# Optimization experiments

Hardware: AMD Instinct MI355X
Metric: run time of the kernel (lower is better)

## Reference

```python
import jax, jax.numpy as jnp
import numpy as np

F, G, S, E, P, B, T = 1024, 512, 512, 256, 8, 256, 256

def _gru(x, h, W_ih, W_hh, b_ih, b_hh):
    # torch.nn.GRUCell math; gate order r, z, n
    gi = x @ W_ih.T + b_ih
    gh = h @ W_hh.T + b_hh
    ir, iz, inn = jnp.split(gi, 3, axis=1)
    hr, hz, hn = jnp.split(gh, 3, axis=1)
    r = jax.nn.sigmoid(ir + hr)
    z = jax.nn.sigmoid(iz + hz)
    n = jnp.tanh(inn + r * hn)
    return (1.0 - z) * n + z * h

def setup_inputs() -> dict:
    key = jax.random.key(0)
    ks = jax.random.split(key, 16)
    feature_ = jax.random.normal(ks[0], (B, F), dtype=jnp.float32)
    spk_id = jax.random.randint(ks[1], (B,), 0, P)
    speaker_mask = jax.nn.one_hot(spk_id, P, dtype=jnp.float32)
    global_history = jax.random.normal(ks[2], (T, B, G), dtype=jnp.float32)
    speaker0 = jax.random.normal(ks[3], (B, P, S), dtype=jnp.float32)
    emotion0 = jax.random.normal(ks[4], (B, E), dtype=jnp.float32)
    sc = 0.05
    return {
        "feature_": feature_, "speaker_mask": speaker_mask,
        "global_history": global_history, "speaker0": speaker0, "emotion0": emotion0,
        "Wg_ih": jax.random.normal(ks[5], (3 * G, F + S)) * sc,
        "Wg_hh": jax.random.normal(ks[6], (3 * G, G)) * sc,
        "bg_ih": jnp.zeros((3 * G,)), "bg_hh": jnp.zeros((3 * G,)),
        "Wp_ih": jax.random.normal(ks[7], (3 * S, F + G)) * sc,
        "Wp_hh": jax.random.normal(ks[8], (3 * S, S)) * sc,
        "bp_ih": jnp.zeros((3 * S,)), "bp_hh": jnp.zeros((3 * S,)),
        "We_ih": jax.random.normal(ks[9], (3 * E, S)) * sc,
        "We_hh": jax.random.normal(ks[10], (3 * E, E)) * sc,
        "be_ih": jnp.zeros((3 * E,)), "be_hh": jnp.zeros((3 * E,)),
        "attn_W": jax.random.normal(ks[11], (G, F)) * sc,
    }

def reference(feature_, speaker_mask, global_history, speaker0, emotion0,
              Wg_ih, Wg_hh, bg_ih, bg_hh,
              Wp_ih, Wp_hh, bp_ih, bp_hh,
              We_ih, We_hh, be_ih, be_hh, attn_W):
    b = feature_.shape[0]
    p = speaker_mask.shape[1]
    spk_id = jnp.argmax(speaker_mask, axis=1)                      # (B,)
    rows = jnp.arange(b)
    sel0 = speaker0[rows, spk_id]                                   # select_parties -> (B, S)
    feature_speak = jnp.concatenate([feature_, sel0], axis=1)       # (B, F+S)
    global_state = _gru(feature_speak, global_history[-1], Wg_ih, Wg_hh, bg_ih, bg_hh)
    # attention over global history (T > 0 path); dropout = identity (eval)
    x_ = feature_ @ attn_W.T                                        # (B, G)
    alpha = jax.nn.softmax(jnp.einsum('bg,tbg->bt', x_, global_history), axis=1)
    context = jnp.einsum('bt,tbg->bg', alpha, global_history)       # (B, G)
    feature_context = jnp.concatenate([feature_, context], axis=1)  # (B, F+G)
    fc = jnp.broadcast_to(feature_context[:, None, :], (b, p, feature_context.shape[1]))
    fc = fc.reshape(b * p, -1)
    parties_state = _gru(fc, speaker0.reshape(b * p, -1), Wp_ih, Wp_hh, bp_ih, bp_hh)
    parties_state = parties_state.reshape(b, p, -1)                 # (B, P, S)
    m = speaker_mask[:, :, None]
    speaker = speaker0 * (1.0 - m) + parties_state * m
    parties = speaker[rows, spk_id]                                 # (B, S)
    emotion = _gru(parties, emotion0, We_ih, We_hh, be_ih, be_hh)
    return emotion, global_state, speaker
```

## Files before the change

kernel.cpp:

```cpp
#include <hip/hip_runtime.h>
#include <hip/hip_bf16.h>
#include <math.h>

#define BB 256
#define FF 1024
#define GG 512
#define SS 512
#define EE 256
#define PP 8
#define TT 256

typedef __attribute__((ext_vector_type(8))) short bs8;
typedef __attribute__((ext_vector_type(4))) float f32x4;

__device__ __forceinline__ float sigmoidf_(float x) { return 1.0f / (1.0f + expf(-x)); }

__device__ __forceinline__ short f2bf(float f) {
    union { float f; unsigned u; } v; v.f = f;
    unsigned r = v.u + 0x7FFFu + ((v.u >> 16) & 1u);
    return (short)(r >> 16);
}

union BPack { bs8 s; __hip_bfloat162 h[4]; };

__device__ __forceinline__ bs8 ld8cvt(const float* p) {
    float4 a = *(const float4*)p, b = *(const float4*)(p + 4);
    BPack u;
    u.h[0] = __float22bfloat162_rn({a.x, a.y});
    u.h[1] = __float22bfloat162_rn({a.z, a.w});
    u.h[2] = __float22bfloat162_rn({b.x, b.y});
    u.h[3] = __float22bfloat162_rn({b.z, b.w});
    return u.s;
}
__device__ __forceinline__ void ld8split(const float* p, bs8& ho, bs8& lo) {
    float4 a = *(const float4*)p, b = *(const float4*)(p + 4);
    float v[8] = {a.x, a.y, a.z, a.w, b.x, b.y, b.z, b.w};
    BPack uh, ul;
#pragma unroll
    for (int j = 0; j < 4; ++j) {
        __hip_bfloat162 h2 = __float22bfloat162_rn({v[2*j], v[2*j+1]});
        uh.h[j] = h2;
        float r0 = v[2*j]   - __low2float(h2);
        float r1 = v[2*j+1] - __high2float(h2);
        ul.h[j] = __float22bfloat162_rn({r0, r1});
    }
    ho = uh.s; lo = ul.s;
}

#define OWG_IH 0L
#define OWG_HH 2359296L
#define OWP_IH 3145728L
#define OWP_HH 5505024L
#define OWE_IH 6291456L
#define OWE_HH 6684672L
#define WTOT   6881280L

#define MB0 0
#define MB1 3360
#define MB2 3616
#define MB3 3744
#define MB4 3808
#define MB5 3840
#define MB6 4096
#define MBE 5120

__global__ __launch_bounds__(256) void k_mega(
        const float* __restrict__ Wg_ih, const float* __restrict__ Wg_hh,
        const float* __restrict__ Wp_ih, const float* __restrict__ Wp_hh,
        const float* __restrict__ We_ih, const float* __restrict__ We_hh,
        const float* __restrict__ attn_W, const float* __restrict__ feature_,
        const float* __restrict__ h_g, const float* __restrict__ emotion0,
        const float* __restrict__ mask, const float* __restrict__ sp0,
        short* __restrict__ Wbf, short* __restrict__ awhi, short* __restrict__ awlo,
        short* __restrict__ xg, short* __restrict__ fhi, short* __restrict__ flo,
        short* __restrict__ hg_bf, short* __restrict__ emo_bf, short* __restrict__ sel0_bf,
        float* __restrict__ sel0, int* __restrict__ spk, float* __restrict__ speaker_out) {
    int blk = blockIdx.x, tid = threadIdx.x;
    if (blk < MB1) {
        long i = (long)blk * 2048 + tid * 8;
        const float* src; long base;
        if      (i < OWG_HH) { src = Wg_ih; base = OWG_IH; }
        else if (i < OWP_IH) { src = Wg_hh; base = OWG_HH; }
        else if (i < OWP_HH) { src = Wp_ih; base = OWP_IH; }
        else if (i < OWE_IH) { src = Wp_hh; base = OWP_HH; }
        else if (i < OWE_HH) { src = We_ih; base = OWE_IH; }
        else                 { src = We_hh; base = OWE_HH; }
        *(bs8*)(Wbf + i) = ld8cvt(src + (i - base));
    } else if (blk < MB2) {
        long i = (long)(blk - MB1) * 2048 + tid * 8;
        bs8 h, l;
        ld8split(attn_W + i, h, l);
        *(bs8*)(awhi + i) = h;
        *(bs8*)(awlo + i) = l;
    } else if (blk < MB3) {
        long i = (long)(blk - MB2) * 2048 + tid * 8;
        bs8 h, l;
        ld8split(feature_ + i, h, l);
        *(bs8*)(fhi + i) = h;
        *(bs8*)(flo + i) = l;
        long b = i >> 10, c = i & 1023;
        *(bs8*)(xg + b * 1536 + c) = h;
    } else if (blk < MB4) {
        long i = (long)(blk - MB3) * 2048 + tid * 8;
        *(bs8*)(hg_bf + i) = ld8cvt(h_g + i);
    } else if (blk < MB5) {
        long i = (long)(blk - MB4) * 2048 + tid * 8;
        *(bs8*)(emo_bf + i) = ld8cvt(emotion0 + i);
    } else if (blk < MB6) {
        int b = blk - MB5;
        __shared__ int sid;
        if (tid == 0) {
            int best = 0; float bv = mask[b * PP];
            for (int p = 1; p < PP; ++p) { float v = mask[b * PP + p]; if (v > bv) { bv = v; best = p; } }
            sid = best; spk[b] = best;
        }
        __syncthreads();
        const float* src = sp0 + ((size_t)b * PP + sid) * SS;
        for (int j = tid; j < SS; j += 256) {
            float v = src[j];
            sel0[(size_t)b * SS + j] = v;
            short h = f2bf(v);
            sel0_bf[(size_t)b * SS + j] = h;
            xg[(size_t)b * 1536 + FF + j] = h;
        }
    } else {
        size_t i = ((size_t)(blk - MB6) * 256 + tid) * 4;
        *(float4*)(speaker_out + i) = *(const float4*)(sp0 + i);
    }
}

struct GDesc {
    const short *A, *A2, *W, *Wl;
    float* C;
    int lda, lda2, kb, ldw, woff, ldc, K, nbn, flags;
};
struct GBatch {
    GDesc d[6];
    int start[7];
    int ng;
};

__global__ __launch_bounds__(256) void k_bgemm(GBatch gb) {
    __shared__ __align__(16) short Ash[64 * 64], Bsh[64 * 64];
    __shared__ __align__(16) short Asl[64 * 64], Bsl[64 * 64];

    int bid = blockIdx.x;
    int g = 0;
    while (g + 1 < gb.ng && bid >= gb.start[g + 1]) ++g;
    GDesc d = gb.d[g];
    int local = bid - gb.start[g];
    int bn = local % d.nbn, bm = local / d.nbn;
    const bool split = (d.flags & 1) != 0;

    const int tid = threadIdx.x;
    const int lane = tid & 63, wid = tid >> 6;
    const int wr = wid >> 1, wc = wid & 1;
    const int r0 = tid >> 3, c0 = tid & 7;
    const int r1 = r0 + 32;
    const int la = lane & 15, lk = lane >> 4;
    const int sw = la & 7;

    f32x4 acc[2][2] = {};

    for (int k0 = 0; k0 < d.K; k0 += 64) {
        bs8 ah0, ah1, bh0, bh1, al0, al1, bl0, bl1;
        if (split) {
            size_t oa0 = (size_t)(bm * 64 + r0) * d.lda + k0 + c0 * 8;
            size_t oa1 = (size_t)(bm * 64 + r1) * d.lda + k0 + c0 * 8;
            size_t ow0 = (size_t)(bn * 64 + r0) * d.ldw + d.woff + k0 + c0 * 8;
            size_t ow1 = (size_t)(bn * 64 + r1) * d.ldw + d.woff + k0 + c0 * 8;
            ah0 = *(const bs8*)(d.A + oa0);  ah1 = *(const bs8*)(d.A + oa1);
            al0 = *(const bs8*)(d.A2 + oa0); al1 = *(const bs8*)(d.A2 + oa1);
            bh0 = *(const bs8*)(d.W + ow0);  bh1 = *(const bs8*)(d.W + ow1);
            bl0 = *(const bs8*)(d.Wl + ow0); bl1 = *(const bs8*)(d.Wl + ow1);
        } else {
            const short* Ab; int alda;
            if (k0 < d.kb) { Ab = d.A + k0; alda = d.lda; }
            else           { Ab = d.A2 + (k0 - d.kb); alda = d.lda2; }
            ah0 = *(const bs8*)(Ab + (size_t)(bm * 64 + r0) * alda + c0 * 8);
            ah1 = *(const bs8*)(Ab + (size_t)(bm * 64 + r1) * alda + c0 * 8);
            bh0 = *(const bs8*)(d.W + (size_t)(bn * 64 + r0) * d.ldw + d.woff + k0 + c0 * 8);
            bh1 = *(const bs8*)(d.W + (size_t)(bn * 64 + r1) * d.ldw + d.woff + k0 + c0 * 8);
        }
        __syncthreads();
        *(bs8*)(Ash + r0 * 64 + ((c0 ^ (r0 & 7)) * 8)) = ah0;
        *(bs8*)(Ash + r1 * 64 + ((c0 ^ (r1 & 7)) * 8)) = ah1;
        *(bs8*)(Bsh + r0 * 64 + ((c0 ^ (r0 & 7)) * 8)) = bh0;
        *(bs8*)(Bsh + r1 * 64 + ((c0 ^ (r1 & 7)) * 8)) = bh1;
        if (split) {
            *(bs8*)(Asl + r0 * 64 + ((c0 ^ (r0 & 7)) * 8)) = al0;
            *(bs8*)(Asl + r1 * 64 + ((c0 ^ (r1 & 7)) * 8)) = al1;
            *(bs8*)(Bsl + r0 * 64 + ((c0 ^ (r0 & 7)) * 8)) = bl0;
            *(bs8*)(Bsl + r1 * 64 + ((c0 ^ (r1 & 7)) * 8)) = bl1;
        }
        __syncthreads();
#pragma unroll
        for (int kk = 0; kk < 2; ++kk) {
            int slot = kk * 4 + lk;
            int off = (slot ^ sw) * 8;
            bs8 a0 = *(const bs8*)(Ash + (wr * 32 + la) * 64      + off);
            bs8 a1 = *(const bs8*)(Ash + (wr * 32 + 16 + la) * 64 + off);
            bs8 b0 = *(const bs8*)(Bsh + (wc * 32 + la) * 64      + off);
            bs8 b1 = *(const bs8*)(Bsh + (wc * 32 + 16 + la) * 64 + off);
            acc[0][0] = __builtin_amdgcn_mfma_f32_16x16x32_bf16(a0, b0, acc[0][0], 0, 0, 0);
            acc[0][1] = __builtin_amdgcn_mfma_f32_16x16x32_bf16(a0, b1, acc[0][1], 0, 0, 0);
            acc[1][0] = __builtin_amdgcn_mfma_f32_16x16x32_bf16(a1, b0, acc[1][0], 0, 0, 0);
            acc[1][1] = __builtin_amdgcn_mfma_f32_16x16x32_bf16(a1, b1, acc[1][1], 0, 0, 0);
            if (split) {
                bs8 xl0 = *(const bs8*)(Asl + (wr * 32 + la) * 64      + off);
                bs8 xl1 = *(const bs8*)(Asl + (wr * 32 + 16 + la) * 64 + off);
                bs8 yl0 = *(const bs8*)(Bsl + (wc * 32 + la) * 64      + off);
                bs8 yl1 = *(const bs8*)(Bsl + (wc * 32 + 16 + la) * 64 + off);
                acc[0][0] = __builtin_amdgcn_mfma_f32_16x16x32_bf16(a0, yl0, acc[0][0], 0, 0, 0);
                acc[0][0] = __builtin_amdgcn_mfma_f32_16x16x32_bf16(xl0, b0, acc[0][0], 0, 0, 0);
                acc[0][1] = __builtin_amdgcn_mfma_f32_16x16x32_bf16(a0, yl1, acc[0][1], 0, 0, 0);
                acc[0][1] = __builtin_amdgcn_mfma_f32_16x16x32_bf16(xl0, b1, acc[0][1], 0, 0, 0);
                acc[1][0] = __builtin_amdgcn_mfma_f32_16x16x32_bf16(a1, yl0, acc[1][0], 0, 0, 0);
                acc[1][0] = __builtin_amdgcn_mfma_f32_16x16x32_bf16(xl1, b0, acc[1][0], 0, 0, 0);
                acc[1][1] = __builtin_amdgcn_mfma_f32_16x16x32_bf16(a1, yl1, acc[1][1], 0, 0, 0);
                acc[1][1] = __builtin_amdgcn_mfma_f32_16x16x32_bf16(xl1, b1, acc[1][1], 0, 0, 0);
            }
        }
    }

    const int rowb = (lane >> 4) * 4, coln = lane & 15;
    const bool accum = (d.flags & 2) != 0;
#pragma unroll
    for (int i = 0; i < 2; ++i)
#pragma unroll
    for (int j = 0; j < 2; ++j)
#pragma unroll
    for (int r = 0; r < 4; ++r) {
        int row = bm * 64 + wr * 32 + i * 16 + rowb + r;
        int col = bn * 64 + wc * 32 + j * 16 + coln;
        size_t idx = (size_t)row * d.ldc + col;
        if (accum) d.C[idx] += acc[i][j][r];
        else       d.C[idx]  = acc[i][j][r];
    }
}

__global__ __launch_bounds__(256) void k_scores(const float* __restrict__ x_,
                                                const float* __restrict__ gh,
                                                float* __restrict__ scores) {
    int task = blockIdx.x * 4 + (threadIdx.x >> 6);
    int lane = threadIdx.x & 63;
    int b = task & (BB - 1), t = task >> 8;
    const float* row = gh + ((size_t)t * BB + b) * GG + lane * 8;
    const float* xb  = x_ + (size_t)b * GG + lane * 8;
    float4 v1 = *(const float4*)row;
    float4 v2 = *(const float4*)(row + 4);
    float4 x1 = *(const float4*)xb;
    float4 x2 = *(const float4*)(xb + 4);
    float p = v1.x*x1.x + v1.y*x1.y + v1.z*x1.z + v1.w*x1.w
            + v2.x*x2.x + v2.y*x2.y + v2.z*x2.z + v2.w*x2.w;
#pragma unroll
    for (int off = 32; off; off >>= 1) p += __shfl_xor(p, off);
    if (lane == 0) scores[b * TT + t] = p;
}

__global__ __launch_bounds__(1024) void k_softctx(const float* __restrict__ scores,
                                                  const float* __restrict__ gh,
                                                  short* __restrict__ ctx_bf) {
    int b = blockIdx.x, tid = threadIdx.x;
    __shared__ float sal[TT];
    __shared__ float red[TT];
    __shared__ float part[16][GG];

    float v = 0.f;
    if (tid < TT) { v = scores[b * TT + tid]; red[tid] = v; }
    __syncthreads();
    for (int off = 128; off; off >>= 1) {
        if (tid < off) red[tid] = fmaxf(red[tid], red[tid + off]);
        __syncthreads();
    }
    float m = red[0];
    __syncthreads();
    float e = 0.f;
    if (tid < TT) { e = expf(v - m); red[tid] = e; }
    __syncthreads();
    for (int off = 128; off; off >>= 1) {
        if (tid < off) red[tid] += red[tid + off];
        __syncthreads();
    }
    if (tid < TT) sal[tid] = e / red[0];
    __syncthreads();

    int w = tid >> 6, lane = tid & 63;
    float acc[8] = {};
    for (int it = 0; it < 16; ++it) {
        int t = w * 16 + it;
        float a = sal[t];
        const float* row = gh + ((size_t)t * BB + b) * GG + lane * 8;
        float4 v1 = *(const float4*)row;
        float4 v2 = *(const float4*)(row + 4);
        acc[0] += a * v1.x; acc[1] += a * v1.y; acc[2] += a * v1.z; acc[3] += a * v1.w;
        acc[4] += a * v2.x; acc[5] += a * v2.y; acc[6] += a * v2.z; acc[7] += a * v2.w;
    }
#pragma unroll
    for (int e2 = 0; e2 < 8; ++e2) part[w][lane * 8 + e2] = acc[e2];
    __syncthreads();
    if (tid < GG) {
        float s = 0.f;
#pragma unroll
        for (int w2 = 0; w2 < 16; ++w2) s += part[w2][tid];
        ctx_bf[(size_t)b * GG + tid] = f2bf(s);
    }
}

__global__ __launch_bounds__(256) void k_gru2(
        const float* __restrict__ gi_g, const float* __restrict__ gh_g,
        const float* __restrict__ bg_ih, const float* __restrict__ bg_hh,
        const float* __restrict__ hg, float* __restrict__ global_out,
        const float* __restrict__ gi_p, const float* __restrict__ gh_p,
        const float* __restrict__ bp_ih, const float* __restrict__ bp_hh,
        const float* __restrict__ sel0, const int* __restrict__ spk,
        short* __restrict__ par_bf, float* __restrict__ speaker_out) {
    int idx = blockIdx.x * 256 + threadIdx.x;
    if (idx < BB * GG) {
        int b = idx / GG, j = idx - b * GG;
        const float* gib = gi_g + (size_t)b * 3 * GG;
        const float* ghb = gh_g + (size_t)b * 3 * GG;
        float r = sigmoidf_(gib[j] + bg_ih[j] + ghb[j] + bg_hh[j]);
        float z = sigmoidf_(gib[GG + j] + bg_ih[GG + j] + ghb[GG + j] + bg_hh[GG + j]);
        float n = tanhf(gib[2*GG + j] + bg_ih[2*GG + j] + r * (ghb[2*GG + j] + bg_hh[2*GG + j]));
        global_out[idx] = (1.0f - z) * n + z * hg[idx];
    } else {
        idx -= BB * GG;
        int b = idx / SS, j = idx - b * SS;
        const float* gib = gi_p + (size_t)b * 3 * SS;
        const float* ghb = gh_p + (size_t)b * 3 * SS;
        float r = sigmoidf_(gib[j] + bp_ih[j] + ghb[j] + bp_hh[j]);
        float z = sigmoidf_(gib[SS + j] + bp_ih[SS + j] + ghb[SS + j] + bp_hh[SS + j]);
        float n = tanhf(gib[2*SS + j] + bp_ih[2*SS + j] + r * (ghb[2*SS + j] + bp_hh[2*SS + j]));
        float o = (1.0f - z) * n + z * sel0[idx];
        par_bf[idx] = f2bf(o);
        speaker_out[((size_t)b * PP + spk[b]) * SS + j] = o;
    }
}

__global__ __launch_bounds__(256) void k_gru(const float* __restrict__ gi, const float* __restrict__ gh,
                                             const float* __restrict__ bih, const float* __restrict__ bhh,
                                             const float* __restrict__ h,
                                             float* __restrict__ out, int H) {
    int idx = blockIdx.x * 256 + threadIdx.x;
    int b = idx / H, j = idx - b * H;
    const float* gib = gi + (size_t)b * 3 * H;
    const float* ghb = gh + (size_t)b * 3 * H;
    float r = sigmoidf_(gib[j] + bih[j] + ghb[j] + bhh[j]);
    float z = sigmoidf_(gib[H + j] + bih[H + j] + ghb[H + j] + bhh[H + j]);
    float n = tanhf(gib[2 * H + j] + bih[2 * H + j] + r * (ghb[2 * H + j] + bhh[2 * H + j]));
    out[idx] = (1.0f - z) * n + z * h[idx];
}

extern "C" void kernel_launch(void* const* d_in, const int* in_sizes, int n_in,
                              void* d_out, int out_size, void* d_ws, size_t ws_size,
                              hipStream_t stream) {
    const float* feature_ = (const float*)d_in[0];
    const float* mask     = (const float*)d_in[1];
    const float* ghist    = (const float*)d_in[2];
    const float* speaker0 = (const float*)d_in[3];
    const float* emotion0 = (const float*)d_in[4];
    const float* Wg_ih    = (const float*)d_in[5];
    const float* Wg_hh    = (const float*)d_in[6];
    const float* bg_ih    = (const float*)d_in[7];
    const float* bg_hh    = (const float*)d_in[8];
    const float* Wp_ih    = (const float*)d_in[9];
    const float* Wp_hh    = (const float*)d_in[10];
    const float* bp_ih    = (const float*)d_in[11];
    const float* bp_hh    = (const float*)d_in[12];
    const float* We_ih    = (const float*)d_in[13];
    const float* We_hh    = (const float*)d_in[14];
    const float* be_ih    = (const float*)d_in[15];
    const float* be_hh    = (const float*)d_in[16];
    const float* attn_W   = (const float*)d_in[17];

    float* out = (float*)d_out;
    float* emotion_out = out;
    float* global_out  = out + (size_t)BB * EE;
    float* speaker_out = global_out + (size_t)BB * GG;

    char* cur = (char*)d_ws;
    short* Wbf     = (short*)cur; cur += (size_t)WTOT * 2;
    short* awhi    = (short*)cur; cur += (size_t)GG * FF * 2;
    short* awlo    = (short*)cur; cur += (size_t)GG * FF * 2;
    short* xg      = (short*)cur; cur += (size_t)BB * 1536 * 2;
    short* fhi     = (short*)cur; cur += (size_t)BB * FF * 2;
    short* flo     = (short*)cur; cur += (size_t)BB * FF * 2;
    short* hg_bf   = (short*)cur; cur += (size_t)BB * GG * 2;
    short* emo_bf  = (short*)cur; cur += (size_t)BB * EE * 2;
    short* sel0_bf = (short*)cur; cur += (size_t)BB * SS * 2;
    short* ctx_bf  = (short*)cur; cur += (size_t)BB * GG * 2;
    short* par_bf  = (short*)cur; cur += (size_t)BB * SS * 2;

    float* sel0    = (float*)cur; cur += (size_t)BB * SS * 4;
    float* x_      = (float*)cur; cur += (size_t)BB * GG * 4;
    float* scores  = (float*)cur; cur += (size_t)BB * TT * 4;
    float* gi_g    = (float*)cur; cur += (size_t)BB * 3 * GG * 4;
    float* gh_g    = (float*)cur; cur += (size_t)BB * 3 * GG * 4;
    float* gi_p    = (float*)cur; cur += (size_t)BB * 3 * SS * 4;
    float* gh_p    = (float*)cur; cur += (size_t)BB * 3 * SS * 4;
    float* gi_e    = (float*)cur; cur += (size_t)BB * 3 * EE * 4;
    float* gh_e    = (float*)cur; cur += (size_t)BB * 3 * EE * 4;
    int*   spk     = (int*)cur;   cur += 256 * 4;

    const float* h_g = ghist + (size_t)(TT - 1) * BB * GG;

    short* Wg_ih_bf = Wbf + OWG_IH;
    short* Wg_hh_bf = Wbf + OWG_HH;
    short* Wp_ih_bf = Wbf + OWP_IH;
    short* Wp_hh_bf = Wbf + OWP_HH;
    short* We_ih_bf = Wbf + OWE_IH;
    short* We_hh_bf = Wbf + OWE_HH;

    k_mega<<<MBE, 256, 0, stream>>>(Wg_ih, Wg_hh, Wp_ih, Wp_hh, We_ih, We_hh,
                                    attn_W, feature_, h_g, emotion0, mask, speaker0,
                                    Wbf, awhi, awlo, xg, fhi, flo, hg_bf, emo_bf,
                                    sel0_bf, sel0, spk, speaker_out);

    GBatch gbA;
    gbA.d[0] = { fhi, flo, awhi, awlo, x_, FF, FF, FF, FF, 0, GG, FF, 8, 1 };
    gbA.d[1] = { xg, xg, Wg_ih_bf, nullptr, gi_g, 1536, 1536, 1536, 1536, 0, 3*GG, 1536, 24, 0 };
    gbA.d[2] = { hg_bf, hg_bf, Wg_hh_bf, nullptr, gh_g, GG, GG, GG, GG, 0, 3*GG, GG, 24, 0 };
    gbA.d[3] = { sel0_bf, sel0_bf, Wp_hh_bf, nullptr, gh_p, SS, SS, SS, SS, 0, 3*SS, SS, 24, 0 };
    gbA.d[4] = { emo_bf, emo_bf, We_hh_bf, nullptr, gh_e, EE, EE, EE, EE, 0, 3*EE, EE, 12, 0 };
    gbA.d[5] = { xg, xg, Wp_ih_bf, nullptr, gi_p, 1536, 1536, 1536, 1536, 0, 3*SS, FF, 24, 0 };
    gbA.start[0] = 0;   gbA.start[1] = 32;  gbA.start[2] = 128; gbA.start[3] = 224;
    gbA.start[4] = 320; gbA.start[5] = 368; gbA.start[6] = 464;
    gbA.ng = 6;
    k_bgemm<<<464, 256, 0, stream>>>(gbA);

    k_scores<<<(BB * TT) / 4, 256, 0, stream>>>(x_, ghist, scores);

    k_softctx<<<BB, 1024, 0, stream>>>(scores, ghist, ctx_bf);

    GBatch gbB;
    gbB.d[0] = { ctx_bf, ctx_bf, Wp_ih_bf, nullptr, gi_p, GG, GG, GG, 1536, FF, 3*SS, GG, 24, 2 };
    gbB.start[0] = 0; gbB.start[1] = 96; gbB.ng = 1;
    k_bgemm<<<96, 256, 0, stream>>>(gbB);

    k_gru2<<<(BB * GG + BB * SS) / 256, 256, 0, stream>>>(
        gi_g, gh_g, bg_ih, bg_hh, h_g, global_out,
        gi_p, gh_p, bp_ih, bp_hh, sel0, spk, par_bf, speaker_out);

    GBatch gbC;
    gbC.d[0] = { par_bf, par_bf, We_ih_bf, nullptr, gi_e, SS, SS, SS, SS, 0, 3*EE, SS, 12, 0 };
    gbC.start[0] = 0; gbC.start[1] = 48; gbC.ng = 1;
    k_bgemm<<<48, 256, 0, stream>>>(gbC);

    k_gru<<<(BB * EE) / 256, 256, 0, stream>>>(gi_e, gh_e, be_ih, be_hh, emotion0, emotion_out, EE);
}
```

Before: 108.7 us.

## Fuse attention scores and context into single-pass split online softmax

Replaces the separate score kernel and softmax/context kernel with a split-T online-softmax kernel that reads each global_history row once, computing scores and weighted accumulation together, followed by a small merge kernel combining 8 chunks per batch row. This removes the second full pass over the large history tensor and increases parallelism from 256 large blocks to 2048 blocks. It adds a partial-context buffer write/read and extra exp work for rescaling.

```diff
diff --git a/kernel.cpp b/kernel.cpp
--- a/kernel.cpp
+++ b/kernel.cpp
@@ -55,7 +55,6 @@
 #define OWE_HH 6684672L
 #define WTOT   6881280L
 
-#define MB0 0
 #define MB1 3360
 #define MB2 3616
 #define MB3 3744
@@ -239,71 +238,85 @@
     }
 }
 
-__global__ __launch_bounds__(256) void k_scores(const float* __restrict__ x_,
-                                                const float* __restrict__ gh,
-                                                float* __restrict__ scores) {
-    int task = blockIdx.x * 4 + (threadIdx.x >> 6);
-    int lane = threadIdx.x & 63;
-    int b = task & (BB - 1), t = task >> 8;
-    const float* row = gh + ((size_t)t * BB + b) * GG + lane * 8;
-    const float* xb  = x_ + (size_t)b * GG + lane * 8;
-    float4 v1 = *(const float4*)row;
-    float4 v2 = *(const float4*)(row + 4);
-    float4 x1 = *(const float4*)xb;
-    float4 x2 = *(const float4*)(xb + 4);
-    float p = v1.x*x1.x + v1.y*x1.y + v1.z*x1.z + v1.w*x1.w
-            + v2.x*x2.x + v2.y*x2.y + v2.z*x2.z + v2.w*x2.w;
-#pragma unroll
-    for (int off = 32; off; off >>= 1) p += __shfl_xor(p, off);
-    if (lane == 0) scores[b * TT + t] = p;
-}
-
-__global__ __launch_bounds__(1024) void k_softctx(const float* __restrict__ scores,
-                                                  const float* __restrict__ gh,
-                                                  short* __restrict__ ctx_bf) {
-    int b = blockIdx.x, tid = threadIdx.x;
-    __shared__ float sal[TT];
-    __shared__ float red[TT];
-    __shared__ float part[16][GG];
-
-    float v = 0.f;
-    if (tid < TT) { v = scores[b * TT + tid]; red[tid] = v; }
-    __syncthreads();
-    for (int off = 128; off; off >>= 1) {
-        if (tid < off) red[tid] = fmaxf(red[tid], red[tid + off]);
-        __syncthreads();
-    }
-    float m = red[0];
-    __syncthreads();
-    float e = 0.f;
-    if (tid < TT) { e = expf(v - m); red[tid] = e; }
-    __syncthreads();
-    for (int off = 128; off; off >>= 1) {
-        if (tid < off) red[tid] += red[tid + off];
-        __syncthreads();
-    }
-    if (tid < TT) sal[tid] = e / red[0];
-    __syncthreads();
-
-    int w = tid >> 6, lane = tid & 63;
+__global__ __launch_bounds__(256) void k_attnp(const float* __restrict__ x_,
+                                               const float* __restrict__ gh,
+                                               float* __restrict__ ctxp,
+                                               float2* __restrict__ msb) {
+    int blk = blockIdx.x;
+    int b = blk & (BB - 1), ch = blk >> 8;
+    int tid = threadIdx.x, w = tid >> 6, lane = tid & 63;
+    __shared__ float wm[4], ws[4];
+    __shared__ float part[4][GG];
+
+    const float* xb = x_ + (size_t)b * GG + lane * 8;
+    float4 xa = *(const float4*)xb;
+    float4 xc = *(const float4*)(xb + 4);
+
+    float m = -INFINITY, s = 0.f;
     float acc[8] = {};
-    for (int it = 0; it < 16; ++it) {
-        int t = w * 16 + it;
-        float a = sal[t];
+    int t0 = ch * 32 + w * 8;
+#pragma unroll
+    for (int it = 0; it < 8; ++it) {
+        int t = t0 + it;
         const float* row = gh + ((size_t)t * BB + b) * GG + lane * 8;
         float4 v1 = *(const float4*)row;
         float4 v2 = *(const float4*)(row + 4);
-        acc[0] += a * v1.x; acc[1] += a * v1.y; acc[2] += a * v1.z; acc[3] += a * v1.w;
-        acc[4] += a * v2.x; acc[5] += a * v2.y; acc[6] += a * v2.z; acc[7] += a * v2.w;
-    }
-#pragma unroll
-    for (int e2 = 0; e2 < 8; ++e2) part[w][lane * 8 + e2] = acc[e2];
+        float p = v1.x*xa.x + v1.y*xa.y + v1.z*xa.z + v1.w*xa.w
+                + v2.x*xc.x + v2.y*xc.y + v2.z*xc.z + v2.w*xc.w;
+#pragma unroll
+        for (int off = 32; off; off >>= 1) p += __shfl_xor(p, off);
+        float nm = fmaxf(m, p);
+        float scale = expf(m - nm);
+        float e = expf(p - nm);
+        s = s * scale + e;
+        acc[0] = acc[0]*scale + e*v1.x; acc[1] = acc[1]*scale + e*v1.y;
+        acc[2] = acc[2]*scale + e*v1.z; acc[3] = acc[3]*scale + e*v1.w;
+        acc[4] = acc[4]*scale + e*v2.x; acc[5] = acc[5]*scale + e*v2.y;
+        acc[6] = acc[6]*scale + e*v2.z; acc[7] = acc[7]*scale + e*v2.w;
+        m = nm;
+    }
+    if (lane == 0) { wm[w] = m; ws[w] = s; }
+    *(float4*)&part[w][lane * 8]     = make_float4(acc[0], acc[1], acc[2], acc[3]);
+    *(float4*)&part[w][lane * 8 + 4] = make_float4(acc[4], acc[5], acc[6], acc[7]);
     __syncthreads();
-    if (tid < GG) {
-        float s = 0.f;
-#pragma unroll
-        for (int w2 = 0; w2 < 16; ++w2) s += part[w2][tid];
-        ctx_bf[(size_t)b * GG + tid] = f2bf(s);
+
+    float M = fmaxf(fmaxf(wm[0], wm[1]), fmaxf(wm[2], wm[3]));
+    float f0 = expf(wm[0] - M), f1 = expf(wm[1] - M);
+    float f2 = expf(wm[2] - M), f3 = expf(wm[3] - M);
+    if (tid == 0) {
+        float S = ws[0]*f0 + ws[1]*f1 + ws[2]*f2 + ws[3]*f3;
+        msb[blk] = make_float2(M, S);
+    }
+    for (int j = tid; j < GG; j += 256) {
+        float r = part[0][j]*f0 + part[1][j]*f1 + part[2][j]*f2 + part[3][j]*f3;
+        ctxp[(size_t)blk * GG + j] = r;
+    }
+}
+
+__global__ __launch_bounds__(256) void k_attnm(const float* __restrict__ ctxp,
+                                               const float2* __restrict__ msb,
+                                               short* __restrict__ ctx_bf) {
+    int b = blockIdx.x, tid = threadIdx.x;
+    float mv[8], sv[8];
+    float M = -INFINITY;
+#pragma unroll
+    for (int c = 0; c < 8; ++c) {
+        float2 t = msb[c * BB + b];
+        mv[c] = t.x; sv[c] = t.y;
+        M = fmaxf(M, t.x);
+    }
+    float S = 0.f;
+    float f[8];
+#pragma unroll
+    for (int c = 0; c < 8; ++c) { f[c] = expf(mv[c] - M); S += sv[c] * f[c]; }
+    float inv = 1.0f / S;
+#pragma unroll
+    for (int c = 0; c < 8; ++c) f[c] *= inv;
+    for (int j = tid; j < GG; j += 256) {
+        float r = 0.f;
+#pragma unroll
+        for (int c = 0; c < 8; ++c) r += ctxp[(size_t)(c * BB + b) * GG + j] * f[c];
+        ctx_bf[(size_t)b * GG + j] = f2bf(r);
     }
 }
 
@@ -394,7 +407,8 @@
 
     float* sel0    = (float*)cur; cur += (size_t)BB * SS * 4;
     float* x_      = (float*)cur; cur += (size_t)BB * GG * 4;
-    float* scores  = (float*)cur; cur += (size_t)BB * TT * 4;
+    float* ctxp    = (float*)cur; cur += (size_t)2048 * GG * 4;
+    float2* msb    = (float2*)cur; cur += (size_t)2048 * 8;
     float* gi_g    = (float*)cur; cur += (size_t)BB * 3 * GG * 4;
     float* gh_g    = (float*)cur; cur += (size_t)BB * 3 * GG * 4;
     float* gi_p    = (float*)cur; cur += (size_t)BB * 3 * SS * 4;
@@ -429,9 +443,9 @@
     gbA.ng = 6;
     k_bgemm<<<464, 256, 0, stream>>>(gbA);
 
-    k_scores<<<(BB * TT) / 4, 256, 0, stream>>>(x_, ghist, scores);
-
-    k_softctx<<<BB, 1024, 0, stream>>>(scores, ghist, ctx_bf);
+    k_attnp<<<2048, 256, 0, stream>>>(x_, ghist, ctxp, msb);
+
+    k_attnm<<<BB, 256, 0, stream>>>(ctxp, msb, ctx_bf);
 
     GBatch gbB;
     gbB.d[0] = { ctx_bf, ctx_bf, Wp_ih_bf, nullptr, gi_p, GG, GG, GG, 1536, FF, 3*SS, GG, 24, 2 };
```

Result: faster. 100.7 us (-7.3%).
